# Optimization experiments

Hardware: AMD Instinct MI355X
Metric: run time of the kernel (lower is better)

The kernel has to match this reference:

```python
import jax, jax.numpy as jnp
import numpy as np

N_USERS = 100000
N_ITEMS = 50000
N_NODES = N_USERS + N_ITEMS
LATENT = 64
NNZ = 2400000
BATCH = 2048
EPS = 1e-12  # F.normalize eps


def setup_inputs() -> dict:
    key = jax.random.key(0)
    ks = jax.random.split(key, 16)
    inp = {
        "rows": jax.random.randint(ks[0], (NNZ,), 0, N_NODES, dtype=jnp.int32),
        "cols": jax.random.randint(ks[1], (NNZ,), 0, N_NODES, dtype=jnp.int32),
        "vals": jax.random.uniform(ks[2], (NNZ,), dtype=jnp.float32),
        "x": jax.random.normal(ks[3], (N_NODES, LATENT), dtype=jnp.float32) * 0.1,
        "users": jax.random.randint(ks[12], (BATCH,), 0, N_USERS, dtype=jnp.int32),
        "items": jax.random.randint(ks[13], (BATCH,), 0, N_ITEMS, dtype=jnp.int32),
    }
    for k in range(2):
        inp[f"W_gc{k}"] = jax.random.normal(ks[4 + 4 * k], (LATENT, LATENT), dtype=jnp.float32) * 0.1
        inp[f"b_gc{k}"] = jax.random.normal(ks[5 + 4 * k], (1, LATENT), dtype=jnp.float32) * 0.1
        inp[f"W_bi{k}"] = jax.random.normal(ks[6 + 4 * k], (LATENT, LATENT), dtype=jnp.float32) * 0.1
        inp[f"b_bi{k}"] = jax.random.normal(ks[7 + 4 * k], (1, LATENT), dtype=jnp.float32) * 0.1
    return inp


def _l2_normalize(v):
    # F.normalize(p=2, dim=1): divide by max(||v||_2, eps)
    n = jnp.sqrt(jnp.sum(v * v, axis=1, keepdims=True))
    return v / jnp.maximum(n, EPS)


def reference(rows, cols, vals, x,
              W_gc0, b_gc0, W_bi0, b_bi0,
              W_gc1, b_gc1, W_bi1, b_bi1,
              users, items):
    weights = [(W_gc0, b_gc0, W_bi0, b_bi0), (W_gc1, b_gc1, W_bi1, b_bi1)]
    ego = x                      # [N, D]
    embs = [x]
    for (Wg, bg, Wb, bb) in weights:
        # sparse adj @ ego  (COO gather + segment-sum scatter)
        msgs = vals[:, None] * ego[cols]                              # [nnz, D]
        side = jax.ops.segment_sum(msgs, rows, num_segments=N_NODES)  # [N, D]
        sum_emb = side @ Wg + bg
        bi_emb = (ego * side) @ Wb + bb
        ego = _l2_normalize(jax.nn.leaky_relu(sum_emb + bi_emb, negative_slope=0.2))
        embs.append(ego)
    all_emb = jnp.concatenate(embs, axis=1)          # [N, 3*D]
    users_emb = all_emb[users]                       # [B, 3*D]
    items_emb = all_emb[N_USERS + items]             # [B, 3*D]
    gamma = jnp.sum(users_emb * items_emb, axis=1)   # [B]
    return gamma
```

## Files before the change

### kernel.cpp

```cpp
#include <hip/hip_runtime.h>

#define N_USERS_C 100000
#define N_NODES_C 150000
#define D 64
#define NB 2344
#define NSUP 74
#define CPAD 16
#define SPAD 68
#define FCAP 1536
#define S1B 256
#define FRAG 240
#define S2CAP 2560
#define BPS 16
#define FPB (S1B / BPS)

__global__ __launch_bounds__(256) void mark1_k(
    const int* __restrict__ u, const int* __restrict__ it,
    unsigned char* __restrict__ samp, unsigned char* __restrict__ need, int batch)
{
    int i = blockIdx.x * blockDim.x + threadIdx.x;
    if (i >= 2 * batch) return;
    int n = (i < batch) ? u[i] : N_USERS_C + it[i - batch];
    samp[n] = 1;
    need[n] = 1;
}

__global__ __launch_bounds__(256) void mark2_k(
    const int* __restrict__ rows, const int* __restrict__ cols,
    const unsigned char* __restrict__ samp, unsigned char* __restrict__ need, int nnz)
{
    int gtid = blockIdx.x * blockDim.x + threadIdx.x;
    int stride = gridDim.x * blockDim.x;
    for (int e = gtid; e < nnz; e += stride)
        if (samp[rows[e]]) need[cols[e]] = 1;
}

__global__ __launch_bounds__(1024) void scan1_k(
    const unsigned char* __restrict__ need, int* __restrict__ part,
    int* __restrict__ bsum, int n)
{
    __shared__ int wsum[16];
    int i = blockIdx.x * 1024 + threadIdx.x;
    int lane = threadIdx.x & 63, wid = threadIdx.x >> 6;
    int v = (i < n) ? (int)need[i] : 0;
    int incl = v;
    #pragma unroll
    for (int off = 1; off < 64; off <<= 1) {
        int t = __shfl_up(incl, off);
        if (lane >= off) incl += t;
    }
    if (lane == 63) wsum[wid] = incl;
    __syncthreads();
    int woff = 0;
    for (int w = 0; w < wid; ++w) woff += wsum[w];
    if (i < n) part[i] = woff + incl - v;
    if (threadIdx.x == 1023) bsum[blockIdx.x] = woff + incl;
}

__global__ __launch_bounds__(1024) void scan2_k(
    int* __restrict__ bsum, int nb, int* __restrict__ Mptr)
{
    __shared__ int wsum[16];
    int lane = threadIdx.x & 63, wid = threadIdx.x >> 6;
    int i = threadIdx.x;
    int v = (i < nb) ? bsum[i] : 0;
    int incl = v;
    #pragma unroll
    for (int off = 1; off < 64; off <<= 1) {
        int t = __shfl_up(incl, off);
        if (lane >= off) incl += t;
    }
    if (lane == 63) wsum[wid] = incl;
    __syncthreads();
    int woff = 0;
    for (int w = 0; w < wid; ++w) woff += wsum[w];
    if (i < nb) bsum[i] = woff + incl - v;
    if (i == nb - 1) Mptr[0] = woff + incl;
}

__global__ __launch_bounds__(256) void scanB_k(
    const int* __restrict__ bsum, int* __restrict__ idx,
    const unsigned char* __restrict__ need, int* __restrict__ list,
    int* __restrict__ bcur, int n)
{
    int i = blockIdx.x * blockDim.x + threadIdx.x;
    if (i < NB) bcur[i * CPAD] = i * FCAP;
    if (i >= n) return;
    int t = idx[i] + bsum[i >> 10];
    if (need[i]) { idx[i] = t; list[t] = i; }
    else idx[i] = -1;
}

__global__ __launch_bounds__(512) void s1_k(
    const int* __restrict__ rows, const int* __restrict__ cols,
    const float* __restrict__ vals, const int* __restrict__ idx,
    int2* __restrict__ pairs1, int* __restrict__ scnt, int nnz)
{
    __shared__ int lcur[NSUP];
    int t = threadIdx.x;
    for (int i = t; i < NSUP; i += 512) lcur[i] = 0;
    __syncthreads();
    int b = blockIdx.x;
    int per = (nnz + S1B - 1) / S1B;
    int s = b * per;
    int e = min(nnz, s + per);
    for (int i = s + t; i < e; i += 512) {
        int ci = idx[rows[i]];
        if (ci < 0) continue;
        int sp = ci >> 11;
        int k = atomicAdd(&lcur[sp], 1);
        pairs1[(size_t)sp * (S1B * FRAG) + b * FRAG + k] =
            make_int2(((ci & 2047) << 18) | cols[i], __float_as_int(vals[i]));
    }
    __syncthreads();
    for (int i = t; i < NSUP; i += 512) scnt[i * S1B + b] = lcur[i];
}

__global__ __launch_bounds__(256) void s2_k(
    const int* __restrict__ scnt, const int2* __restrict__ pairs1,
    int* __restrict__ bcurP, int2* __restrict__ pairs)
{
    __shared__ int2 sbuf[S2CAP];
    __shared__ int fcnt[32], fcur[32], gb[32];
    int sp = blockIdx.x / BPS, part = blockIdx.x % BPS;
    int t = threadIdx.x;
    if (t < 32) { fcnt[t] = 0; fcur[t] = 0; }
    __syncthreads();
    int base = 0;
    for (int fi = 0; fi < FPB; ++fi) {
        int b = part * FPB + fi;
        int m = scnt[sp * S1B + b];
        const int2* src = &pairs1[(size_t)sp * (S1B * FRAG) + b * FRAG];
        for (int i = t; i < m; i += 256) {
            int2 p = src[i];
            sbuf[base + i] = p;
            atomicAdd(&fcnt[(p.x >> 18) >> 6], 1);
        }
        base += m;
    }
    __syncthreads();
    if (t < 32) {
        int c = fcnt[t];
        gb[t] = c ? atomicAdd(&bcurP[(sp * 32 + t) * CPAD], c) : 0;
    }
    __syncthreads();
    for (int i = t; i < base; i += 256) {
        int2 p = sbuf[i];
        int ris = p.x >> 18;
        int f = ris >> 6;
        int k = atomicAdd(&fcur[f], 1);
        pairs[gb[f] + k] = make_int2(((ris & 63) << 18) | (p.x & 0x3FFFF), p.y);
    }
}

__global__ __launch_bounds__(256) void sortb_k(
    const int* __restrict__ bcurP, int2* __restrict__ pairs,
    int* __restrict__ rp)
{
    __shared__ int2 buf[FCAP];
    __shared__ int cnt[64];
    __shared__ int cur[64];
    int b = blockIdx.x;
    int s = b * FCAP;
    int e = bcurP[b * CPAD];
    int m = e - s;
    int t = threadIdx.x;
    if (t < 64) cnt[t] = 0;
    __syncthreads();
    for (int i = t; i < m; i += 256) {
        int2 p = pairs[s + i];
        buf[i] = p;
        atomicAdd(&cnt[p.x >> 18], 1);
    }
    __syncthreads();
    if (t < 64) {
        int v = cnt[t];
        int incl = v;
        #pragma unroll
        for (int o = 1; o < 64; o <<= 1) {
            int u = __shfl_up(incl, o);
            if (t >= o) incl += u;
        }
        cur[t] = incl - v;
        rp[b * 65 + t] = s + incl - v;
        if (t == 63) rp[b * 65 + 64] = s + incl;
    }
    __syncthreads();
    for (int i = t; i < m; i += 256) {
        int2 p = buf[i];
        int dst = atomicAdd(&cur[p.x >> 18], 1);
        pairs[s + dst] = make_int2(p.x & 0x3FFFF, p.y);
    }
}

__global__ __launch_bounds__(256) void gather1_k(
    const int* __restrict__ rp, const int2* __restrict__ pairs,
    const float* __restrict__ x, float* __restrict__ side,
    const int* __restrict__ Mptr)
{
    int gtid = blockIdx.x * blockDim.x + threadIdx.x;
    int wave = gtid >> 6;
    int lane = threadIdx.x & 63;
    if (wave >= Mptr[0]) return;
    int rb = (wave >> 6) * 65 + (wave & 63);
    int s  = rp[rb];
    int ep = rp[rb + 1];

    float acc = 0.0f;
    for (int base = s; base < ep; base += 64) {
        int2 p = make_int2(0, 0);
        if (base + lane < ep) p = pairs[base + lane];
        int cnt8 = (min(ep - base, 64) + 7) & ~7;
        for (int j = 0; j < cnt8; j += 8) {
            int cc[8]; float vv[8], ff[8];
            #pragma unroll
            for (int q = 0; q < 8; ++q) {
                cc[q] = __shfl(p.x, j + q);
                vv[q] = __int_as_float(__shfl(p.y, j + q));
            }
            #pragma unroll
            for (int q = 0; q < 8; ++q)
                ff[q] = x[(size_t)cc[q] * D + lane];
            #pragma unroll
            for (int q = 0; q < 8; ++q)
                acc = fmaf(vv[q], ff[q], acc);
        }
    }
    side[(size_t)wave * D + lane] = acc;
}

__global__ __launch_bounds__(256) void gather2_k(
    const int* __restrict__ rp, const int2* __restrict__ pairs,
    const float* __restrict__ e1c, const int* __restrict__ idx,
    float* __restrict__ side2c, float* __restrict__ egoc,
    const int* __restrict__ u, const int* __restrict__ it, int batch)
{
    int gtid = blockIdx.x * blockDim.x + threadIdx.x;
    int wave = gtid >> 6;
    int lane = threadIdx.x & 63;
    if (wave >= 2 * batch) return;
    int n = (wave < batch) ? u[wave] : N_USERS_C + it[wave - batch];
    int cr = idx[n];
    int rb = (cr >> 6) * 65 + (cr & 63);
    int s  = rp[rb];
    int ep = rp[rb + 1];

    float acc = 0.0f;
    for (int base = s; base < ep; base += 64) {
        int2 p = make_int2(0, 0);
        if (base + lane < ep) p = pairs[base + lane];
        int cnt = min(ep - base, 64);
        for (int j = 0; j < cnt; ++j) {
            int   c = __shfl(p.x, j);
            float v = __int_as_float(__shfl(p.y, j));
            acc = fmaf(v, e1c[(size_t)idx[c] * D + lane], acc);
        }
    }
    side2c[(size_t)wave * D + lane] = acc;
    egoc[(size_t)wave * D + lane] = e1c[(size_t)cr * D + lane];
}

__global__ __launch_bounds__(256) void transform_k(
    const float* __restrict__ S, const float* __restrict__ Eb,
    const float* __restrict__ Wg, const float* __restrict__ bg,
    const float* __restrict__ Wb, const float* __restrict__ bb,
    float* __restrict__ out, const int* __restrict__ list,
    const int* __restrict__ Mptr, int nrows)
{
    __shared__ __align__(16) float sWg[D * D];
    __shared__ __align__(16) float sWb[D * D];
    __shared__ __align__(16) float sAT[D][SPAD];
    __shared__ __align__(16) float sBT[D][SPAD];

    int nr = Mptr ? Mptr[0] : nrows;
    int t  = threadIdx.x;
    int tc = t & 15;
    int tr = t >> 4;
    int r0 = blockIdx.x * 64;
    if (r0 >= nr) return;

    for (int i = t; i < D * D; i += 256) {
        sWg[i] = Wg[i];
        sWb[i] = Wb[i];
    }
    for (int itr = 0; itr < 4; ++itr) {
        int rr  = itr * 16 + (t >> 4);
        int row = r0 + rr;
        float4 sv = make_float4(0.f, 0.f, 0.f, 0.f);
        float4 ev = sv;
        if (row < nr) {
            sv = *(const float4*)&S[(size_t)row * D + tc * 4];
            int er = list ? list[row] : row;
            ev = *(const float4*)&Eb[(size_t)er * D + tc * 4];
        }
        sAT[tc * 4 + 0][rr] = sv.x;
        sAT[tc * 4 + 1][rr] = sv.y;
        sAT[tc * 4 + 2][rr] = sv.z;
        sAT[tc * 4 + 3][rr] = sv.w;
        sBT[tc * 4 + 0][rr] = sv.x * ev.x;
        sBT[tc * 4 + 1][rr] = sv.y * ev.y;
        sBT[tc * 4 + 2][rr] = sv.z * ev.z;
        sBT[tc * 4 + 3][rr] = sv.w * ev.w;
    }
    __syncthreads();

    float acc[4][4] = {};
    for (int k = 0; k < D; ++k) {
        float4 a4 = *(const float4*)&sAT[k][tr * 4];
        float4 b4 = *(const float4*)&sBT[k][tr * 4];
        float4 g4 = *(const float4*)&sWg[k * D + tc * 4];
        float4 w4 = *(const float4*)&sWb[k * D + tc * 4];
        float av[4] = {a4.x, a4.y, a4.z, a4.w};
        float bv[4] = {b4.x, b4.y, b4.z, b4.w};
        float gv[4] = {g4.x, g4.y, g4.z, g4.w};
        float wv[4] = {w4.x, w4.y, w4.z, w4.w};
        #pragma unroll
        for (int i = 0; i < 4; ++i)
            #pragma unroll
            for (int j = 0; j < 4; ++j)
                acc[i][j] = fmaf(av[i], gv[j], fmaf(bv[i], wv[j], acc[i][j]));
    }

    float4 bgv = *(const float4*)&bg[tc * 4];
    float4 bbv = *(const float4*)&bb[tc * 4];
    float bias[4] = {bgv.x + bbv.x, bgv.y + bbv.y, bgv.z + bbv.z, bgv.w + bbv.w};

    float vv[4][4];
    float ss[4] = {0.f, 0.f, 0.f, 0.f};
    #pragma unroll
    for (int i = 0; i < 4; ++i) {
        #pragma unroll
        for (int j = 0; j < 4; ++j) {
            float v = acc[i][j] + bias[j];
            v = (v > 0.0f) ? v : 0.2f * v;
            vv[i][j] = v;
            ss[i] += v * v;
        }
    }
    #pragma unroll
    for (int i = 0; i < 4; ++i) {
        #pragma unroll
        for (int off = 1; off < 16; off <<= 1)
            ss[i] += __shfl_xor(ss[i], off);
    }
    #pragma unroll
    for (int i = 0; i < 4; ++i) {
        int row = r0 + tr * 4 + i;
        if (row < nr) {
            float inv = 1.0f / fmaxf(sqrtf(ss[i]), 1e-12f);
            float4 o = make_float4(vv[i][0] * inv, vv[i][1] * inv,
                                   vv[i][2] * inv, vv[i][3] * inv);
            *(float4*)&out[(size_t)row * D + tc * 4] = o;
        }
    }
}

__global__ __launch_bounds__(256) void gamma_k(
    const float* __restrict__ x, const float* __restrict__ e1c,
    const int* __restrict__ idx, const float* __restrict__ e2c,
    const int* __restrict__ users, const int* __restrict__ items,
    float* __restrict__ gamma, int batch)
{
    int gtid = blockIdx.x * blockDim.x + threadIdx.x;
    int wave = gtid >> 6;
    int lane = threadIdx.x & 63;
    if (wave >= batch) return;
    size_t uu = (size_t)users[wave];
    size_t tt = (size_t)(N_USERS_C + items[wave]);
    float acc = x[uu * D + lane] * x[tt * D + lane]
              + e1c[(size_t)idx[uu] * D + lane] * e1c[(size_t)idx[tt] * D + lane]
              + e2c[(size_t)wave * D + lane] * e2c[(size_t)(batch + wave) * D + lane];
    #pragma unroll
    for (int off = 1; off < 64; off <<= 1) acc += __shfl_xor(acc, off);
    if (lane == 0) gamma[wave] = acc;
}

extern "C" void kernel_launch(void* const* d_in, const int* in_sizes, int n_in,
                              void* d_out, int out_size, void* d_ws, size_t ws_size,
                              hipStream_t stream) {
    const int*   rows  = (const int*)d_in[0];
    const int*   cols  = (const int*)d_in[1];
    const float* vals  = (const float*)d_in[2];
    const float* x     = (const float*)d_in[3];
    const int*   users = (const int*)d_in[4];
    const int*   items = (const int*)d_in[5];
    const float* Wg0 = (const float*)d_in[6];
    const float* bg0 = (const float*)d_in[7];
    const float* Wb0 = (const float*)d_in[8];
    const float* bb0 = (const float*)d_in[9];
    const float* Wg1 = (const float*)d_in[10];
    const float* bg1 = (const float*)d_in[11];
    const float* Wb1 = (const float*)d_in[12];
    const float* bb1 = (const float*)d_in[13];

    int nnz   = in_sizes[0];
    int batch = in_sizes[4];
    float* out = (float*)d_out;

    size_t emb = (size_t)N_NODES_C * D;
    float* A      = (float*)d_ws;
    float* Sbuf   = A + emb;
    int*   bcur   = (int*)(Sbuf + emb);
    int*   rp     = bcur + NB * CPAD;
    int*   idx    = rp + NB * 65 + 2;
    int*   list   = idx + N_NODES_C;
    int*   bsum   = list + N_NODES_C;
    int*   Mptr   = bsum + 1024;
    int*   scnt   = Mptr + 4;
    unsigned char* need = (unsigned char*)(scnt + NSUP * S1B);
    unsigned char* samp = need + N_NODES_C;
    int2*  pairs  = (int2*)(((size_t)(samp + N_NODES_C) + 15) & ~(size_t)15);

    int2*  pairs1 = (int2*)Sbuf;
    float* side2c = Sbuf;
    float* egoc   = Sbuf + (size_t)2 * 2048 * D;
    float* e2c    = egoc + (size_t)2 * 2048 * D;

    int nscan = (N_NODES_C + 1023) / 1024;

    hipMemsetAsync(need, 0, 2 * N_NODES_C, stream);
    mark1_k<<<(2 * batch + 255) / 256, 256, 0, stream>>>(users, items, samp, need, batch);
    mark2_k<<<1024, 256, 0, stream>>>(rows, cols, samp, need, nnz);
    scan1_k<<<nscan, 1024, 0, stream>>>(need, idx, bsum, N_NODES_C);
    scan2_k<<<1, 1024, 0, stream>>>(bsum, nscan, Mptr);
    scanB_k<<<(N_NODES_C + 255) / 256, 256, 0, stream>>>(bsum, idx, need, list, bcur, N_NODES_C);

    s1_k<<<S1B, 512, 0, stream>>>(rows, cols, vals, idx, pairs1, scnt, nnz);
    s2_k<<<NSUP * BPS, 256, 0, stream>>>(scnt, pairs1, bcur, pairs);
    sortb_k<<<NB, 256, 0, stream>>>(bcur, pairs, rp);

    gather1_k<<<(N_NODES_C * 64 + 255) / 256, 256, 0, stream>>>(
        rp, pairs, x, Sbuf, Mptr);
    transform_k<<<(N_NODES_C + 63) / 64, 256, 0, stream>>>(
        Sbuf, x, Wg0, bg0, Wb0, bb0, A, list, Mptr, 0);

    gather2_k<<<(2 * batch * 64 + 255) / 256, 256, 0, stream>>>(
        rp, pairs, A, idx, side2c, egoc, users, items, batch);
    transform_k<<<(2 * batch + 63) / 64, 256, 0, stream>>>(
        side2c, egoc, Wg1, bg1, Wb1, bb1, e2c, nullptr, nullptr, 2 * batch);

    gamma_k<<<(batch * 64 + 255) / 256, 256, 0, stream>>>(
        x, A, idx, e2c, users, items, out, batch);
}
```

Before: 277.5 us.

## Process four rows per wave with float4 gathers; fold block-sum scan into scanB

Both SpMM gather kernels now give each 16-lane quarter-wave its own row and load float4 slices of the source embeddings, instead of one wave per row loading one float per lane. This is meant to cut wasted shuffles and issue wider, fewer memory loads, since average row length is about 16 nonzeros. The separate single-block scan2 kernel is removed, and every scanB block recomputes the 147-entry block prefix serially in shared memory, saving one launch at the cost of redundant per-block work. Loop trip counts are now set by the longest row among the four, so lanes with shorter rows may sit idle.

New measurement: 262.1 us. -5.5%, faster.

```diff
diff --git a/kernel.cpp b/kernel.cpp
--- a/kernel.cpp
+++ b/kernel.cpp
@@ -13,6 +13,7 @@
 #define S2CAP 2560
 #define BPS 16
 #define FPB (S1B / BPS)
+#define NSCAN 147
 
 __global__ __launch_bounds__(256) void mark1_k(
     const int* __restrict__ u, const int* __restrict__ it,
@@ -57,37 +58,28 @@
     if (threadIdx.x == 1023) bsum[blockIdx.x] = woff + incl;
 }
 
-__global__ __launch_bounds__(1024) void scan2_k(
-    int* __restrict__ bsum, int nb, int* __restrict__ Mptr)
-{
-    __shared__ int wsum[16];
-    int lane = threadIdx.x & 63, wid = threadIdx.x >> 6;
-    int i = threadIdx.x;
-    int v = (i < nb) ? bsum[i] : 0;
-    int incl = v;
-    #pragma unroll
-    for (int off = 1; off < 64; off <<= 1) {
-        int t = __shfl_up(incl, off);
-        if (lane >= off) incl += t;
-    }
-    if (lane == 63) wsum[wid] = incl;
-    __syncthreads();
-    int woff = 0;
-    for (int w = 0; w < wid; ++w) woff += wsum[w];
-    if (i < nb) bsum[i] = woff + incl - v;
-    if (i == nb - 1) Mptr[0] = woff + incl;
-}
-
 __global__ __launch_bounds__(256) void scanB_k(
     const int* __restrict__ bsum, int* __restrict__ idx,
     const unsigned char* __restrict__ need, int* __restrict__ list,
-    int* __restrict__ bcur, int n)
-{
-    int i = blockIdx.x * blockDim.x + threadIdx.x;
+    int* __restrict__ bcur, int* __restrict__ Mptr, int n)
+{
+    __shared__ int pre[NSCAN + 1];
+    int t = threadIdx.x;
+    __shared__ int raw[NSCAN];
+    if (t < NSCAN) raw[t] = bsum[t];
+    __syncthreads();
+    if (t == 0) {
+        int run = 0;
+        for (int k = 0; k < NSCAN; ++k) { pre[k] = run; run += raw[k]; }
+        pre[NSCAN] = run;
+    }
+    __syncthreads();
+    int i = blockIdx.x * blockDim.x + t;
     if (i < NB) bcur[i * CPAD] = i * FCAP;
+    if (blockIdx.x == 0 && t == 0) Mptr[0] = pre[NSCAN];
     if (i >= n) return;
-    int t = idx[i] + bsum[i >> 10];
-    if (need[i]) { idx[i] = t; list[t] = i; }
+    int val = idx[i] + pre[i >> 10];
+    if (need[i]) { idx[i] = val; list[val] = i; }
     else idx[i] = -1;
 }
 
@@ -201,32 +193,53 @@
     int gtid = blockIdx.x * blockDim.x + threadIdx.x;
     int wave = gtid >> 6;
     int lane = threadIdx.x & 63;
-    if (wave >= Mptr[0]) return;
-    int rb = (wave >> 6) * 65 + (wave & 63);
-    int s  = rp[rb];
-    int ep = rp[rb + 1];
-
-    float acc = 0.0f;
-    for (int base = s; base < ep; base += 64) {
+    int M = Mptr[0];
+    if (wave * 4 >= M) return;
+    int lq = lane & 15;
+    int qb = lane & 48;
+    int row = wave * 4 + (lane >> 4);
+    int valid = row < M;
+    int s = 0, len = 0;
+    if (valid) {
+        int rb = (row >> 6) * 65 + (row & 63);
+        s = rp[rb];
+        len = rp[rb + 1] - s;
+    }
+    int ml = len;
+    ml = max(ml, __shfl_xor(ml, 16));
+    ml = max(ml, __shfl_xor(ml, 32));
+
+    float4 acc = make_float4(0.f, 0.f, 0.f, 0.f);
+    for (int base = 0; base < ml; base += 16) {
         int2 p = make_int2(0, 0);
-        if (base + lane < ep) p = pairs[base + lane];
-        int cnt8 = (min(ep - base, 64) + 7) & ~7;
-        for (int j = 0; j < cnt8; j += 8) {
-            int cc[8]; float vv[8], ff[8];
-            #pragma unroll
-            for (int q = 0; q < 8; ++q) {
-                cc[q] = __shfl(p.x, j + q);
-                vv[q] = __int_as_float(__shfl(p.y, j + q));
+        int o = base + lq;
+        if (o < len) p = pairs[s + o];
+        int rem = len - base;
+        rem = min(max(rem, 0), 16);
+        int mr = rem;
+        mr = max(mr, __shfl_xor(mr, 16));
+        mr = max(mr, __shfl_xor(mr, 32));
+        int cnt4 = (mr + 3) & ~3;
+        for (int j = 0; j < cnt4; j += 4) {
+            int c[4]; float v[4]; float4 f[4];
+            #pragma unroll
+            for (int q = 0; q < 4; ++q) {
+                c[q] = __shfl(p.x, qb | (j + q));
+                v[q] = __int_as_float(__shfl(p.y, qb | (j + q)));
             }
             #pragma unroll
-            for (int q = 0; q < 8; ++q)
-                ff[q] = x[(size_t)cc[q] * D + lane];
-            #pragma unroll
-            for (int q = 0; q < 8; ++q)
-                acc = fmaf(vv[q], ff[q], acc);
-        }
-    }
-    side[(size_t)wave * D + lane] = acc;
+            for (int q = 0; q < 4; ++q)
+                f[q] = *(const float4*)&x[(size_t)c[q] * D + lq * 4];
+            #pragma unroll
+            for (int q = 0; q < 4; ++q) {
+                acc.x = fmaf(v[q], f[q].x, acc.x);
+                acc.y = fmaf(v[q], f[q].y, acc.y);
+                acc.z = fmaf(v[q], f[q].z, acc.z);
+                acc.w = fmaf(v[q], f[q].w, acc.w);
+            }
+        }
+    }
+    if (valid) *(float4*)&side[(size_t)row * D + lq * 4] = acc;
 }
 
 __global__ __launch_bounds__(256) void gather2_k(
@@ -238,26 +251,62 @@
     int gtid = blockIdx.x * blockDim.x + threadIdx.x;
     int wave = gtid >> 6;
     int lane = threadIdx.x & 63;
-    if (wave >= 2 * batch) return;
-    int n = (wave < batch) ? u[wave] : N_USERS_C + it[wave - batch];
-    int cr = idx[n];
-    int rb = (cr >> 6) * 65 + (cr & 63);
-    int s  = rp[rb];
-    int ep = rp[rb + 1];
-
-    float acc = 0.0f;
-    for (int base = s; base < ep; base += 64) {
+    int nr = 2 * batch;
+    if (wave * 4 >= nr) return;
+    int lq = lane & 15;
+    int qb = lane & 48;
+    int r = wave * 4 + (lane >> 4);
+    int valid = r < nr;
+    int s = 0, len = 0, cr = 0;
+    if (valid) {
+        int n = (r < batch) ? u[r] : N_USERS_C + it[r - batch];
+        cr = idx[n];
+        int rb = (cr >> 6) * 65 + (cr & 63);
+        s = rp[rb];
+        len = rp[rb + 1] - s;
+    }
+    int ml = len;
+    ml = max(ml, __shfl_xor(ml, 16));
+    ml = max(ml, __shfl_xor(ml, 32));
+
+    float4 acc = make_float4(0.f, 0.f, 0.f, 0.f);
+    for (int base = 0; base < ml; base += 16) {
         int2 p = make_int2(0, 0);
-        if (base + lane < ep) p = pairs[base + lane];
-        int cnt = min(ep - base, 64);
-        for (int j = 0; j < cnt; ++j) {
-            int   c = __shfl(p.x, j);
-            float v = __int_as_float(__shfl(p.y, j));
-            acc = fmaf(v, e1c[(size_t)idx[c] * D + lane], acc);
-        }
-    }
-    side2c[(size_t)wave * D + lane] = acc;
-    egoc[(size_t)wave * D + lane] = e1c[(size_t)cr * D + lane];
+        int o = base + lq;
+        if (o < len) p = pairs[s + o];
+        int rem = len - base;
+        rem = min(max(rem, 0), 16);
+        int mr = rem;
+        mr = max(mr, __shfl_xor(mr, 16));
+        mr = max(mr, __shfl_xor(mr, 32));
+        int cnt4 = (mr + 3) & ~3;
+        for (int j = 0; j < cnt4; j += 4) {
+            int c[4]; float v[4]; float4 f[4];
+            #pragma unroll
+            for (int q = 0; q < 4; ++q) {
+                c[q] = __shfl(p.x, qb | (j + q));
+                v[q] = __int_as_float(__shfl(p.y, qb | (j + q)));
+            }
+            #pragma unroll
+            for (int q = 0; q < 4; ++q) {
+                int cc = idx[c[q]];
+                cc = max(cc, 0);
+                f[q] = *(const float4*)&e1c[(size_t)cc * D + lq * 4];
+            }
+            #pragma unroll
+            for (int q = 0; q < 4; ++q) {
+                acc.x = fmaf(v[q], f[q].x, acc.x);
+                acc.y = fmaf(v[q], f[q].y, acc.y);
+                acc.z = fmaf(v[q], f[q].z, acc.z);
+                acc.w = fmaf(v[q], f[q].w, acc.w);
+            }
+        }
+    }
+    if (valid) {
+        *(float4*)&side2c[(size_t)r * D + lq * 4] = acc;
+        *(float4*)&egoc[(size_t)r * D + lq * 4] =
+            *(const float4*)&e1c[(size_t)cr * D + lq * 4];
+    }
 }
 
 __global__ __launch_bounds__(256) void transform_k(
@@ -416,25 +465,22 @@
     float* egoc   = Sbuf + (size_t)2 * 2048 * D;
     float* e2c    = egoc + (size_t)2 * 2048 * D;
 
-    int nscan = (N_NODES_C + 1023) / 1024;
-
     hipMemsetAsync(need, 0, 2 * N_NODES_C, stream);
     mark1_k<<<(2 * batch + 255) / 256, 256, 0, stream>>>(users, items, samp, need, batch);
     mark2_k<<<1024, 256, 0, stream>>>(rows, cols, samp, need, nnz);
-    scan1_k<<<nscan, 1024, 0, stream>>>(need, idx, bsum, N_NODES_C);
-    scan2_k<<<1, 1024, 0, stream>>>(bsum, nscan, Mptr);
-    scanB_k<<<(N_NODES_C + 255) / 256, 256, 0, stream>>>(bsum, idx, need, list, bcur, N_NODES_C);
+    scan1_k<<<NSCAN, 1024, 0, stream>>>(need, idx, bsum, N_NODES_C);
+    scanB_k<<<(N_NODES_C + 255) / 256, 256, 0, stream>>>(bsum, idx, need, list, bcur, Mptr, N_NODES_C);
 
     s1_k<<<S1B, 512, 0, stream>>>(rows, cols, vals, idx, pairs1, scnt, nnz);
     s2_k<<<NSUP * BPS, 256, 0, stream>>>(scnt, pairs1, bcur, pairs);
     sortb_k<<<NB, 256, 0, stream>>>(bcur, pairs, rp);
 
-    gather1_k<<<(N_NODES_C * 64 + 255) / 256, 256, 0, stream>>>(
+    gather1_k<<<(N_NODES_C / 4 * 64 + 255) / 256, 256, 0, stream>>>(
         rp, pairs, x, Sbuf, Mptr);
     transform_k<<<(N_NODES_C + 63) / 64, 256, 0, stream>>>(
         Sbuf, x, Wg0, bg0, Wb0, bb0, A, list, Mptr, 0);
 
-    gather2_k<<<(2 * batch * 64 + 255) / 256, 256, 0, stream>>>(
+    gather2_k<<<(2 * batch / 4 * 64 + 255) / 256, 256, 0, stream>>>(
         rp, pairs, A, idx, side2c, egoc, users, items, batch);
     transform_k<<<(2 * batch + 63) / 64, 256, 0, stream>>>(
         side2c, egoc, Wg1, bg1, Wb1, bb1, e2c, nullptr, nullptr, 2 * batch);
```
